# Performance work log

Measured on AMD Instinct MI355X. Metric: run time of the kernel, lower is better.

Reference implementation:

```python
import jax, jax.numpy as jnp
import numpy as np

BN_EPS = 1e-5


def setup_inputs() -> dict:
    key = jax.random.key(0)
    ks = jax.random.split(key, 4)
    B, C, N = 16, 512, 4096
    Cr = C // 4
    x = jax.random.normal(ks[0], (B, C, N), dtype=jnp.float32)
    W1 = jax.random.normal(ks[1], (Cr, C), dtype=jnp.float32) * (1.0 / np.sqrt(C))
    W2 = jax.random.normal(ks[2], (C, Cr), dtype=jnp.float32) * (1.0 / np.sqrt(Cr))
    gamma = jnp.ones((Cr,), dtype=jnp.float32)
    beta = jnp.zeros((Cr,), dtype=jnp.float32)
    running_mean = jnp.zeros((Cr,), dtype=jnp.float32)
    running_var = jnp.ones((Cr,), dtype=jnp.float32)
    return {"x": x, "W1": W1, "gamma": gamma, "beta": beta,
            "running_mean": running_mean, "running_var": running_var, "W2": W2}


def reference(x, W1, gamma, beta, running_mean, running_var, W2):
    # att[b,c] = sum_j (x x^T)[b,c,j] = sum_n x[b,c,n] * s[b,n], s = colsum over channels.
    # Algebraically identical to bmm(x, x^T).sum(-1), avoids the [B,C,C] intermediate.
    s = jnp.sum(x, axis=1)                       # [B, N]
    att = jnp.einsum('bcn,bn->bc', x, s)         # [B, C]
    # 1x1 Conv1d (no bias) on a length-1 sequence == dense matmul.
    h = jnp.einsum('oc,bc->bo', W1, att)         # [B, C/4]
    # BatchNorm1d (inference mode, running statistics)
    h = gamma * (h - running_mean) * jax.lax.rsqrt(running_var + BN_EPS) + beta
    h = jax.nn.relu(h)
    a = jax.nn.sigmoid(jnp.einsum('oc,bc->bo', W2, h))  # [B, C]
    return x * a[:, :, None]                     # [B, C, N]
```

## Files before the change

kernel.cpp:

```cpp
#include <hip/hip_runtime.h>
#include <math.h>

#define B_   16
#define C_   512
#define CR_  128
#define N_   4096
#define N4_  (N_ / 4)
#define TN   32
#define TN4  (TN / 4)
#define SUBT 4
#define NTB  (N_ / TN / SUBT)

static constexpr float BN_EPS_F = 1e-5f;

typedef float vfloat4 __attribute__((ext_vector_type(4)));

__global__ __launch_bounds__(256) void k1f_att(
        const float* __restrict__ x,
        float* __restrict__ att_part) {
    const int ntb = blockIdx.x;
    const int b   = blockIdx.y;
    const int t   = threadIdx.x;
    const int g   = t >> 3;
    const int i   = t & 7;

    __shared__ vfloat4 s_red[32][8];
    __shared__ vfloat4 s_tile4[8];
    __shared__ float   att_s[C_];

    att_s[t] = 0.f;
    att_s[t + 256] = 0.f;

    const vfloat4* x4 = (const vfloat4*)x;

    for (int sub = 0; sub < SUBT; ++sub) {
        const int nt = ntb * SUBT + sub;
        const vfloat4* base = x4 + (size_t)b * C_ * N4_ + (size_t)nt * TN4;
        vfloat4 v[16];
        vfloat4 sacc = {0.f, 0.f, 0.f, 0.f};
#pragma unroll
        for (int st = 0; st < 16; ++st) {
            v[st] = base[(size_t)(st * 32 + g) * N4_ + i];
            sacc += v[st];
        }
        __syncthreads();
        s_red[g][i] = sacc;
        __syncthreads();
        if (t < 8) {
            vfloat4 acc = {0.f, 0.f, 0.f, 0.f};
#pragma unroll
            for (int g2 = 0; g2 < 32; ++g2)
                acc += s_red[g2][t];
            s_tile4[t] = acc;
        }
        __syncthreads();
        const vfloat4 sv = s_tile4[i];
#pragma unroll
        for (int st = 0; st < 16; ++st) {
            float d = v[st].x * sv.x + v[st].y * sv.y
                    + v[st].z * sv.z + v[st].w * sv.w;
            d += __shfl_xor(d, 1, 64);
            d += __shfl_xor(d, 2, 64);
            d += __shfl_xor(d, 4, 64);
            if (i == 0) att_s[st * 32 + g] += d;
        }
    }
    __syncthreads();
    float* dst = att_part + ((size_t)ntb * B_ + b) * C_;
    dst[t]       = att_s[t];
    dst[t + 256] = att_s[t + 256];
}

__global__ void k3f(const float* __restrict__ att_part,
                    const float* __restrict__ W1,
                    const float* __restrict__ gamma,
                    const float* __restrict__ beta,
                    const float* __restrict__ rmean,
                    const float* __restrict__ rvar,
                    const float* __restrict__ W2,
                    float* __restrict__ a) {
    __shared__ float att_s[C_];
    __shared__ float h_s[CR_];
    const int b = blockIdx.x;
    const int t = threadIdx.x;

    {
        float a0 = 0.f, a1 = 0.f;
#pragma unroll 8
        for (int nb = 0; nb < NTB; ++nb) {
            const float* p = att_part + ((size_t)nb * B_ + b) * C_;
            a0 += p[t];
            a1 += p[t + 256];
        }
        att_s[t]       = a0;
        att_s[t + 256] = a1;
    }
    __syncthreads();

    if (t < CR_) {
        const float* w = W1 + (size_t)t * C_;
        float a0 = 0.f, a1 = 0.f, a2 = 0.f, a3 = 0.f;
#pragma unroll 4
        for (int c = 0; c < C_; c += 4) {
            a0 += w[c + 0] * att_s[c + 0];
            a1 += w[c + 1] * att_s[c + 1];
            a2 += w[c + 2] * att_s[c + 2];
            a3 += w[c + 3] * att_s[c + 3];
        }
        float acc = (a0 + a1) + (a2 + a3);
        float vv = gamma[t] * (acc - rmean[t]) * rsqrtf(rvar[t] + BN_EPS_F) + beta[t];
        h_s[t] = fmaxf(vv, 0.f);
    }
    __syncthreads();
#pragma unroll
    for (int j0 = 0; j0 < C_; j0 += 256) {
        const int j = j0 + t;
        const float* w = W2 + (size_t)j * CR_;
        float a0 = 0.f, a1 = 0.f, a2 = 0.f, a3 = 0.f;
#pragma unroll 4
        for (int k = 0; k < CR_; k += 4) {
            a0 += w[k + 0] * h_s[k + 0];
            a1 += w[k + 1] * h_s[k + 1];
            a2 += w[k + 2] * h_s[k + 2];
            a3 += w[k + 3] * h_s[k + 3];
        }
        float acc = (a0 + a1) + (a2 + a3);
        a[(size_t)b * C_ + j] = 1.f / (1.f + expf(-acc));
    }
}

__global__ void k4_scale(const float* __restrict__ x,
                         const float* __restrict__ a,
                         float* __restrict__ out) {
    const size_t total4 = (size_t)B_ * C_ * N_ / 4;
    const size_t stride = (size_t)gridDim.x * blockDim.x;
    for (size_t idx = (size_t)blockIdx.x * blockDim.x + threadIdx.x;
         idx < total4; idx += stride) {
        const size_t row = idx >> 10;
        const float av = a[row];
        vfloat4 xv = ((const vfloat4*)x)[idx];
        vfloat4 ov = xv * av;
        __builtin_nontemporal_store(ov, &((vfloat4*)out)[idx]);
    }
}

extern "C" void kernel_launch(void* const* d_in, const int* in_sizes, int n_in,
                              void* d_out, int out_size, void* d_ws, size_t ws_size,
                              hipStream_t stream) {
    const float* x     = (const float*)d_in[0];
    const float* W1    = (const float*)d_in[1];
    const float* gamma = (const float*)d_in[2];
    const float* beta  = (const float*)d_in[3];
    const float* rmean = (const float*)d_in[4];
    const float* rvar  = (const float*)d_in[5];
    const float* W2    = (const float*)d_in[6];
    float* out = (float*)d_out;

    float* ws       = (float*)d_ws;
    float* att_part = ws;
    float* a        = att_part + (size_t)NTB * B_ * C_;

    k1f_att<<<dim3(NTB, B_), 256, 0, stream>>>(x, att_part);
    k3f<<<dim3(B_), 256, 0, stream>>>(att_part, W1, gamma, beta, rmean, rvar, W2, a);
    k4_scale<<<dim3(2048), 256, 0, stream>>>(x, a, out);
}
```

Baseline: 90.33 us.

## Accumulate per-channel dots in registers, halve sub-tiles, one block per row in scale

The attention kernel now keeps per-channel dot-product partials in registers across sub-tiles and does a single shuffle reduction and direct global write at the end. This removes the shared-memory accumulator and the per-subtile shuffles. SUBT drops from 4 to 2, which doubles the number of blocks and partial rows that k3f must sum. The scale kernel switches from a grid-stride loop to one block per row with an unrolled loop, so the scale factor is loaded once per block.

```diff
diff --git a/kernel.cpp b/kernel.cpp
--- a/kernel.cpp
+++ b/kernel.cpp
@@ -8,7 +8,7 @@
 #define N4_  (N_ / 4)
 #define TN   32
 #define TN4  (TN / 4)
-#define SUBT 4
+#define SUBT 2
 #define NTB  (N_ / TN / SUBT)
 
 static constexpr float BN_EPS_F = 1e-5f;
@@ -26,12 +26,11 @@
 
     __shared__ vfloat4 s_red[32][8];
     __shared__ vfloat4 s_tile4[8];
-    __shared__ float   att_s[C_];
-
-    att_s[t] = 0.f;
-    att_s[t + 256] = 0.f;
 
     const vfloat4* x4 = (const vfloat4*)x;
+    float dacc[16];
+#pragma unroll
+    for (int st = 0; st < 16; ++st) dacc[st] = 0.f;
 
     for (int sub = 0; sub < SUBT; ++sub) {
         const int nt = ntb * SUBT + sub;
@@ -43,7 +42,7 @@
             v[st] = base[(size_t)(st * 32 + g) * N4_ + i];
             sacc += v[st];
         }
-        __syncthreads();
+        if (sub) __syncthreads();
         s_red[g][i] = sacc;
         __syncthreads();
         if (t < 8) {
@@ -56,19 +55,25 @@
         __syncthreads();
         const vfloat4 sv = s_tile4[i];
 #pragma unroll
-        for (int st = 0; st < 16; ++st) {
-            float d = v[st].x * sv.x + v[st].y * sv.y
-                    + v[st].z * sv.z + v[st].w * sv.w;
-            d += __shfl_xor(d, 1, 64);
-            d += __shfl_xor(d, 2, 64);
-            d += __shfl_xor(d, 4, 64);
-            if (i == 0) att_s[st * 32 + g] += d;
-        }
+        for (int st = 0; st < 16; ++st)
+            dacc[st] += v[st].x * sv.x + v[st].y * sv.y
+                      + v[st].z * sv.z + v[st].w * sv.w;
     }
-    __syncthreads();
-    float* dst = att_part + ((size_t)ntb * B_ + b) * C_;
-    dst[t]       = att_s[t];
-    dst[t + 256] = att_s[t + 256];
+
+#pragma unroll
+    for (int st = 0; st < 16; ++st) {
+        float d = dacc[st];
+        d += __shfl_xor(d, 1, 64);
+        d += __shfl_xor(d, 2, 64);
+        d += __shfl_xor(d, 4, 64);
+        dacc[st] = d;
+    }
+    if (i == 0) {
+        float* dst = att_part + ((size_t)ntb * B_ + b) * C_;
+#pragma unroll
+        for (int st = 0; st < 16; ++st)
+            dst[st * 32 + g] = dacc[st];
+    }
 }
 
 __global__ void k3f(const float* __restrict__ att_part,
@@ -129,18 +134,19 @@
     }
 }
 
-__global__ void k4_scale(const float* __restrict__ x,
-                         const float* __restrict__ a,
-                         float* __restrict__ out) {
-    const size_t total4 = (size_t)B_ * C_ * N_ / 4;
-    const size_t stride = (size_t)gridDim.x * blockDim.x;
-    for (size_t idx = (size_t)blockIdx.x * blockDim.x + threadIdx.x;
-         idx < total4; idx += stride) {
-        const size_t row = idx >> 10;
-        const float av = a[row];
-        vfloat4 xv = ((const vfloat4*)x)[idx];
-        vfloat4 ov = xv * av;
-        __builtin_nontemporal_store(ov, &((vfloat4*)out)[idx]);
+__global__ __launch_bounds__(256) void k4_scale(
+        const float* __restrict__ x,
+        const float* __restrict__ a,
+        float* __restrict__ out) {
+    const int row = blockIdx.x;
+    const float av = a[row];
+    const vfloat4* xr = (const vfloat4*)x + (size_t)row * N4_;
+    vfloat4* orow     = (vfloat4*)out     + (size_t)row * N4_;
+#pragma unroll
+    for (int it = 0; it < N4_ / 256; ++it) {
+        const int idx = it * 256 + threadIdx.x;
+        vfloat4 ov = xr[idx] * av;
+        __builtin_nontemporal_store(ov, &orow[idx]);
     }
 }
 
@@ -162,5 +168,5 @@
 
     k1f_att<<<dim3(NTB, B_), 256, 0, stream>>>(x, att_part);
     k3f<<<dim3(B_), 256, 0, stream>>>(att_part, W1, gamma, beta, rmean, rvar, W2, a);
-    k4_scale<<<dim3(2048), 256, 0, stream>>>(x, a, out);
+    k4_scale<<<dim3(B_ * C_), 256, 0, stream>>>(x, a, out);
 }
```

Measured after the change: 88.29 us. 1.02x faster.
